# Performance work log

Hardware: AMD Instinct MI355X
Metric: run time of the kernel (lower is better)

## Reference

```python
import jax, jax.numpy as jnp
import numpy as np

N, E = 50000, 250000          # nodes, edges
IN, OUT, EDIM = 9, 84, 1      # NNConv(9, 84), edge nn Linear(1, 9*84)
EPS = 1e-5                    # BatchNorm1d default eps


def setup_inputs() -> dict:
    key = jax.random.key(0)
    ks = jax.random.split(key, 8)
    return {
        "x": jax.random.normal(ks[0], (N, IN), jnp.float32),
        "edge_index": jax.random.randint(ks[1], (2, E), 0, N, dtype=jnp.int64),
        "edge_attr": jax.random.normal(ks[2], (E, EDIM), jnp.float32),
        # edge nn: Linear(EDIM, IN*OUT) generating per-edge weight matrices
        "nn_w": jax.random.normal(ks[3], (EDIM, IN * OUT), jnp.float32) * (1.0 / np.sqrt(EDIM)),
        "nn_b": jnp.zeros((IN * OUT,), jnp.float32),
        # NNConv root weight + bias
        "root": jax.random.normal(ks[4], (IN, OUT), jnp.float32) * (1.0 / np.sqrt(IN)),
        "bias": jnp.zeros((OUT,), jnp.float32),
        # BatchNorm1d(84) affine params
        "gamma": jnp.ones((OUT,), jnp.float32),
        "beta": jnp.zeros((OUT,), jnp.float32),
    }


def reference(x, edge_index, edge_attr, nn_w, nn_b, root, bias, gamma, beta):
    src, dst = edge_index[0], edge_index[1]
    # per-edge weight matrices: [E, IN, OUT]
    w_e = (edge_attr @ nn_w + nn_b).reshape(E, IN, OUT)
    # gather source node features and apply edge-specific matmul: [E, OUT]
    msg = jnp.einsum('ei,eio->eo', x[src], w_e)
    # scatter-add to destination nodes (NNConv default aggr='add'): [N, OUT]
    aggr = jax.ops.segment_sum(msg, dst, num_segments=N)
    out = x @ root + aggr + bias
    # BatchNorm1d(84), training mode (biased batch stats)
    mean = out.mean(0)
    var = out.var(0)
    out = (out - mean) * jax.lax.rsqrt(var + EPS) * gamma + beta
    return out
```

## Files before the change

kernel.cpp:

```cpp
#include <hip/hip_runtime.h>

#define N_NODES 50000
#define E_EDGES 250000
#define IN_F 9
#define OUT_F 84
#define GROUPS 21
#define BN_EPS 1e-5f

#define NB_TILE 48
#define NTILES ((N_NODES + NB_TILE - 1) / NB_TILE)
#define NCOPIES 32
#define CAP 32

#define VDIM 27
#define NPAIR 378
#define NM 405
#define SLEN 408
#define VSTR 52
#define NSLOT 196

#define FB_TILE 96
#define FB_NT ((N_NODES + FB_TILE - 1) / FB_TILE)
#define VTS 28

#define CNT_OFF   0
#define STATC_OFF 50048
#define ZERO_WORDS 63104
#define SLOT_OFF  63232
#define SX_OFF    3263232
#define SS_OFF    4663232

__global__ __launch_bounds__(256)
void fill_slots_kernel(const int* __restrict__ ei,
                       const float* __restrict__ ea,
                       int* __restrict__ cnt,
                       int2* __restrict__ slot) {
    int e = (blockIdx.x * blockDim.x + threadIdx.x) * 4;
    if (e < E_EDGES) {
        int4   s4 = *(const int4*)&ei[e];
        int4   d4 = *(const int4*)&ei[E_EDGES + e];
        float4 a4 = *(const float4*)&ea[e];
        int pos;
        pos = atomicAdd(&cnt[d4.x], 1);
        if (pos < CAP) slot[d4.x * CAP + pos] = make_int2(s4.x, __float_as_int(a4.x));
        pos = atomicAdd(&cnt[d4.y], 1);
        if (pos < CAP) slot[d4.y * CAP + pos] = make_int2(s4.y, __float_as_int(a4.y));
        pos = atomicAdd(&cnt[d4.z], 1);
        if (pos < CAP) slot[d4.z * CAP + pos] = make_int2(s4.z, __float_as_int(a4.z));
        pos = atomicAdd(&cnt[d4.w], 1);
        if (pos < CAP) slot[d4.w * CAP + pos] = make_int2(s4.w, __float_as_int(a4.w));
    }
}

__global__ void gather_gram_kernel(const float* __restrict__ x,
                                   const int*   __restrict__ cnt,
                                   const int2*  __restrict__ slot,
                                   float* __restrict__ SX,
                                   float* __restrict__ statc) {
    __shared__ __align__(16) float V[VDIM * VSTR];
    __shared__ __align__(16) int2 rec[NB_TILE][CAP];
    __shared__ int cnt_s[NB_TILE];
    __shared__ unsigned char sI[NSLOT], sJ[NSLOT];

    const int tid = threadIdx.x;
    const int nbase = blockIdx.x * NB_TILE;

    for (int t = tid; t < NSLOT; t += blockDim.x) {
        int tt = t, i = 0;
        while (tt >= ((VDIM - i + 1) >> 1)) { tt -= (VDIM - i + 1) >> 1; ++i; }
        sI[t] = (unsigned char)i;
        sJ[t] = (unsigned char)(i + 2 * tt);
    }
    for (int t = tid; t < VDIM * 4; t += blockDim.x)
        V[(t >> 2) * VSTR + NB_TILE + (t & 3)] = 0.f;
    if (tid < NB_TILE) {
        int n = nbase + tid;
        int c = (n < N_NODES) ? cnt[n] : 0;
        cnt_s[tid] = (c > CAP) ? CAP : c;
    }
    __syncthreads();

    if (tid < NB_TILE * 4) {
        int nl = tid >> 2, part = tid & 3;
        int c = cnt_s[nl];
        const int4* grow = (const int4*)&slot[(nbase + nl) * CAP];
        int4* lrow = (int4*)&rec[nl][0];
#pragma unroll
        for (int j = 0; j < 4; ++j) {
            int s = part * 8 + j * 2;
            if (s < c) lrow[part * 4 + j] = grow[part * 4 + j];
        }
    }
    __syncthreads();

    for (int it = tid; it < NB_TILE * IN_F; it += blockDim.x) {
        int nl = it / IN_F, i = it - nl * IN_F;
        int n = nbase + nl;
        float xv = 0.f, s0 = 0.f, s1 = 0.f;
        if (n < N_NODES) {
            xv = x[n * IN_F + i];
            int c = cnt_s[nl];
            const int2* r = rec[nl];
            int k = 0;
            for (; k + 4 <= c; k += 4) {
                int2 r0 = r[k], r1 = r[k+1], r2 = r[k+2], r3 = r[k+3];
                float a0 = x[r0.x * IN_F + i];
                float a1 = x[r1.x * IN_F + i];
                float a2 = x[r2.x * IN_F + i];
                float a3 = x[r3.x * IN_F + i];
                s0 += (a0 + a1) + (a2 + a3);
                s1 += __int_as_float(r0.y) * a0 + __int_as_float(r1.y) * a1
                    + __int_as_float(r2.y) * a2 + __int_as_float(r3.y) * a3;
            }
            for (; k < c; ++k) {
                int2 r0 = r[k];
                float a0 = x[r0.x * IN_F + i];
                s0 += a0;
                s1 += __int_as_float(r0.y) * a0;
            }
            float* sx = SX + n * VTS;
            sx[i]      = xv;
            sx[9 + i]  = s0;
            sx[18 + i] = s1;
        }
        V[i * VSTR + nl]        = xv;
        V[(9 + i) * VSTR + nl]  = s0;
        V[(18 + i) * VSTR + nl] = s1;
    }
    __syncthreads();

    float* sc = statc + (blockIdx.x & (NCOPIES - 1)) * SLEN;
    for (int t = tid; t < NSLOT + VDIM; t += blockDim.x) {
        if (t < NSLOT) {
            int i = sI[t], j0 = sJ[t];
            int h2 = (j0 < VDIM - 1);
            const float4* vi = (const float4*)&V[i * VSTR];
            const float4* va = (const float4*)&V[j0 * VSTR];
            const float4* vb = (const float4*)&V[(j0 + h2) * VSTR];
            float acc0 = 0.f, acc1 = 0.f;
#pragma unroll
            for (int m = 0; m < VSTR / 4; ++m) {
                float4 a = vi[m], p = va[m], q = vb[m];
                acc0 += a.x * p.x + a.y * p.y + a.z * p.z + a.w * p.w;
                acc1 += a.x * q.x + a.y * q.y + a.z * q.z + a.w * q.w;
            }
            int base = i * VDIM - (i * (i - 1)) / 2;
            atomicAdd(&sc[base + (j0 - i)], acc0);
            if (h2) atomicAdd(&sc[base + (j0 - i) + 1], acc1);
        } else {
            int r = t - NSLOT;
            const float4* vi = (const float4*)&V[r * VSTR];
            float acc = 0.f;
#pragma unroll
            for (int m = 0; m < VSTR / 4; ++m) {
                float4 a = vi[m];
                acc += (a.x + a.y) + (a.z + a.w);
            }
            atomicAdd(&sc[NPAIR + r], acc);
        }
    }
}

__global__ __launch_bounds__(256)
void scale_kernel(const float* __restrict__ nw,
                  const float* __restrict__ nb,
                  const float* __restrict__ root,
                  const float* __restrict__ bias,
                  const float* __restrict__ gamma,
                  const float* __restrict__ beta,
                  const float* __restrict__ statc,
                  float* __restrict__ ss) {
    __shared__ float M[NM];
    const int tid = threadIdx.x;
    for (int t = tid; t < NM; t += blockDim.x) {
        float a = 0.f;
#pragma unroll
        for (int c = 0; c < NCOPIES; ++c) a += statc[c * SLEN + t];
        M[t] = a;
    }
    __syncthreads();
    if (tid < OUT_F) {
        const int o = tid;
        float c[VDIM];
#pragma unroll
        for (int i = 0; i < IN_F; ++i) {
            c[i]      = root[i * OUT_F + o];
            c[9 + i]  = nb[i * OUT_F + o];
            c[18 + i] = nw[i * OUT_F + o];
        }
        float sv = 0.f;
#pragma unroll
        for (int i = 0; i < VDIM; ++i) sv += M[NPAIR + i] * c[i];
        float q = 0.f;
        int t2 = 0;
        for (int i = 0; i < VDIM; ++i) {
            q += c[i] * c[i] * M[t2++];
            for (int j = i + 1; j < VDIM; ++j)
                q += 2.f * c[i] * c[j] * M[t2++];
        }
        const float b = bias[o];
        const float inv_n = 1.0f / (float)N_NODES;
        float mean  = (sv + (float)N_NODES * b) * inv_n;
        float sumsq = q + 2.f * b * sv + (float)N_NODES * b * b;
        float var   = sumsq * inv_n - mean * mean;
        float scl   = rsqrtf(var + BN_EPS) * gamma[o];
        ss[o]         = scl;
        ss[OUT_F + o] = beta[o] - mean * scl;
    }
}

__global__ __launch_bounds__(256, 2)
void final_kernel(const float* __restrict__ SX,
                  const float* __restrict__ nw,
                  const float* __restrict__ nb,
                  const float* __restrict__ root,
                  const float* __restrict__ bias,
                  const float* __restrict__ ss,
                  float* __restrict__ out) {
    __shared__ __align__(16) float4 Ws[IN_F * GROUPS];
    __shared__ __align__(16) float4 Bs[IN_F * GROUPS];
    __shared__ __align__(16) float4 Rs[IN_F * GROUPS];
    __shared__ __align__(16) float Vt[FB_TILE * VTS];

    const int tid = threadIdx.x;
    const int nbase = blockIdx.x * FB_TILE;
    const int nn = (N_NODES - nbase < FB_TILE) ? (N_NODES - nbase) : FB_TILE;

    for (int t = tid; t < IN_F * GROUPS; t += blockDim.x) {
        Ws[t] = ((const float4*)nw)[t];
        Bs[t] = ((const float4*)nb)[t];
        Rs[t] = ((const float4*)root)[t];
    }

    {
        const float4* sx4 = (const float4*)(SX + nbase * VTS);
        float4* vt4 = (float4*)Vt;
        const int nf4 = (nn * VTS) >> 2;
        for (int f = tid; f < nf4; f += blockDim.x)
            vt4[f] = sx4[f];
    }
    __syncthreads();

    const int g = tid % GROUPS;
    const int lane = tid / GROUPS;
    if (tid < 252) {
        float4 C[27];
#pragma unroll
        for (int i = 0; i < IN_F; ++i) {
            C[i]      = Rs[i * GROUPS + g];
            C[9 + i]  = Bs[i * GROUPS + g];
            C[18 + i] = Ws[i * GROUPS + g];
        }
        const float4 b4  = ((const float4*)bias)[g];
        const float4 sc4 = ((const float4*)ss)[g];
        const float4 sh4 = ((const float4*)(ss + OUT_F))[g];
#pragma unroll
        for (int k = 0; k < 8; ++k) {
            const int nl = k * 12 + lane;
            const int n  = nbase + nl;
            if (n < N_NODES) {
                const float* vr = &Vt[nl * VTS];
                float4 a0 = *(const float4*)(vr + 0);
                float4 a1 = *(const float4*)(vr + 4);
                float4 a2 = *(const float4*)(vr + 8);
                float4 a3 = *(const float4*)(vr + 12);
                float4 a4 = *(const float4*)(vr + 16);
                float4 a5 = *(const float4*)(vr + 20);
                float4 a6 = *(const float4*)(vr + 24);
                float4 acc = b4;
#define ACC(VC, IDX)                                                      \
                acc.x += (VC) * C[IDX].x;                                 \
                acc.y += (VC) * C[IDX].y;                                 \
                acc.z += (VC) * C[IDX].z;                                 \
                acc.w += (VC) * C[IDX].w;
                ACC(a0.x, 0)  ACC(a0.y, 1)  ACC(a0.z, 2)  ACC(a0.w, 3)
                ACC(a1.x, 4)  ACC(a1.y, 5)  ACC(a1.z, 6)  ACC(a1.w, 7)
                ACC(a2.x, 8)  ACC(a2.y, 9)  ACC(a2.z, 10) ACC(a2.w, 11)
                ACC(a3.x, 12) ACC(a3.y, 13) ACC(a3.z, 14) ACC(a3.w, 15)
                ACC(a4.x, 16) ACC(a4.y, 17) ACC(a4.z, 18) ACC(a4.w, 19)
                ACC(a5.x, 20) ACC(a5.y, 21) ACC(a5.z, 22) ACC(a5.w, 23)
                ACC(a6.x, 24) ACC(a6.y, 25) ACC(a6.z, 26)
#undef ACC
                acc.x = acc.x * sc4.x + sh4.x;
                acc.y = acc.y * sc4.y + sh4.y;
                acc.z = acc.z * sc4.z + sh4.z;
                acc.w = acc.w * sc4.w + sh4.w;
                *(float4*)&out[n * OUT_F + g * 4] = acc;
            }
        }
    }
}

extern "C" void kernel_launch(void* const* d_in, const int* in_sizes, int n_in,
                              void* d_out, int out_size, void* d_ws, size_t ws_size,
                              hipStream_t stream) {
    const float* x     = (const float*)d_in[0];
    const int*   ei    = (const int*)d_in[1];
    const float* ea    = (const float*)d_in[2];
    const float* nw    = (const float*)d_in[3];
    const float* nb    = (const float*)d_in[4];
    const float* root  = (const float*)d_in[5];
    const float* bias  = (const float*)d_in[6];
    const float* gamma = (const float*)d_in[7];
    const float* beta  = (const float*)d_in[8];
    float*       out   = (float*)d_out;

    float* wsf   = (float*)d_ws;
    int*   wsi   = (int*)d_ws;
    int*   cnt   = wsi + CNT_OFF;
    float* statc = wsf + STATC_OFF;
    int2*  slot  = (int2*)(wsi + SLOT_OFF);
    float* SX    = wsf + SX_OFF;
    float* ss    = wsf + SS_OFF;

    hipMemsetAsync(wsi, 0, ZERO_WORDS * sizeof(int), stream);
    fill_slots_kernel<<<(E_EDGES / 4 + 255) / 256, 256, 0, stream>>>(ei, ea, cnt, slot);
    gather_gram_kernel<<<NTILES, 256, 0, stream>>>(x, cnt, slot, SX, statc);
    scale_kernel<<<1, 256, 0, stream>>>(nw, nb, root, bias, gamma, beta, statc, ss);
    final_kernel<<<FB_NT, 256, 0, stream>>>(SX, nw, nb, root, bias, ss, out);
}
```

Baseline: 116.6 us.

## Pad x to 12 floats for float4 neighbor gathers and enlarge node tile

```diff
diff --git a/kernel.cpp b/kernel.cpp
--- a/kernel.cpp
+++ b/kernel.cpp
@@ -7,8 +7,6 @@
 #define GROUPS 21
 #define BN_EPS 1e-5f
 
-#define NB_TILE 48
-#define NTILES ((N_NODES + NB_TILE - 1) / NB_TILE)
 #define NCOPIES 32
 #define CAP 32
 
@@ -16,12 +14,18 @@
 #define NPAIR 378
 #define NM 405
 #define SLEN 408
-#define VSTR 52
 #define NSLOT 196
+
+#define NB2 96
+#define NT2 ((N_NODES + NB2 - 1) / NB2)
+#define VSTR2 100
 
 #define FB_TILE 96
 #define FB_NT ((N_NODES + FB_TILE - 1) / FB_TILE)
 #define VTS 28
+
+#define EB ((E_EDGES / 4 + 255) / 256)
+#define XB ((N_NODES + 255) / 256)
 
 #define CNT_OFF   0
 #define STATC_OFF 50048
@@ -29,41 +33,56 @@
 #define SLOT_OFF  63232
 #define SX_OFF    3263232
 #define SS_OFF    4663232
+#define XP_OFF    4663408
 
 __global__ __launch_bounds__(256)
 void fill_slots_kernel(const int* __restrict__ ei,
                        const float* __restrict__ ea,
+                       const float* __restrict__ x,
                        int* __restrict__ cnt,
-                       int2* __restrict__ slot) {
-    int e = (blockIdx.x * blockDim.x + threadIdx.x) * 4;
-    if (e < E_EDGES) {
-        int4   s4 = *(const int4*)&ei[e];
-        int4   d4 = *(const int4*)&ei[E_EDGES + e];
-        float4 a4 = *(const float4*)&ea[e];
-        int pos;
-        pos = atomicAdd(&cnt[d4.x], 1);
-        if (pos < CAP) slot[d4.x * CAP + pos] = make_int2(s4.x, __float_as_int(a4.x));
-        pos = atomicAdd(&cnt[d4.y], 1);
-        if (pos < CAP) slot[d4.y * CAP + pos] = make_int2(s4.y, __float_as_int(a4.y));
-        pos = atomicAdd(&cnt[d4.z], 1);
-        if (pos < CAP) slot[d4.z * CAP + pos] = make_int2(s4.z, __float_as_int(a4.z));
-        pos = atomicAdd(&cnt[d4.w], 1);
-        if (pos < CAP) slot[d4.w * CAP + pos] = make_int2(s4.w, __float_as_int(a4.w));
-    }
-}
-
-__global__ void gather_gram_kernel(const float* __restrict__ x,
-                                   const int*   __restrict__ cnt,
-                                   const int2*  __restrict__ slot,
-                                   float* __restrict__ SX,
-                                   float* __restrict__ statc) {
-    __shared__ __align__(16) float V[VDIM * VSTR];
-    __shared__ __align__(16) int2 rec[NB_TILE][CAP];
-    __shared__ int cnt_s[NB_TILE];
+                       int2* __restrict__ slot,
+                       float* __restrict__ xp) {
+    const int bx = blockIdx.x, tid = threadIdx.x;
+    if (bx < EB) {
+        int e = (bx * 256 + tid) * 4;
+        if (e < E_EDGES) {
+            int4   s4 = *(const int4*)&ei[e];
+            int4   d4 = *(const int4*)&ei[E_EDGES + e];
+            float4 a4 = *(const float4*)&ea[e];
+            int pos;
+            pos = atomicAdd(&cnt[d4.x], 1);
+            if (pos < CAP) slot[d4.x * CAP + pos] = make_int2(s4.x, __float_as_int(a4.x));
+            pos = atomicAdd(&cnt[d4.y], 1);
+            if (pos < CAP) slot[d4.y * CAP + pos] = make_int2(s4.y, __float_as_int(a4.y));
+            pos = atomicAdd(&cnt[d4.z], 1);
+            if (pos < CAP) slot[d4.z * CAP + pos] = make_int2(s4.z, __float_as_int(a4.z));
+            pos = atomicAdd(&cnt[d4.w], 1);
+            if (pos < CAP) slot[d4.w * CAP + pos] = make_int2(s4.w, __float_as_int(a4.w));
+        }
+    } else {
+        int n = (bx - EB) * 256 + tid;
+        if (n < N_NODES) {
+            const float* xr = x + n * IN_F;
+            float4* xd = (float4*)&xp[n * 12];
+            xd[0] = make_float4(xr[0], xr[1], xr[2], xr[3]);
+            xd[1] = make_float4(xr[4], xr[5], xr[6], xr[7]);
+            xd[2] = make_float4(xr[8], 0.f, 0.f, 0.f);
+        }
+    }
+}
+
+__global__ __launch_bounds__(256)
+void gather_gram_kernel(const float* __restrict__ xp,
+                        const int*   __restrict__ cnt,
+                        const int2*  __restrict__ slot,
+                        float* __restrict__ SX,
+                        float* __restrict__ statc) {
+    __shared__ __align__(16) float V[VDIM * VSTR2];
+    __shared__ int cnt_s[NB2];
     __shared__ unsigned char sI[NSLOT], sJ[NSLOT];
 
     const int tid = threadIdx.x;
-    const int nbase = blockIdx.x * NB_TILE;
+    const int nbase = blockIdx.x * NB2;
 
     for (int t = tid; t < NSLOT; t += blockDim.x) {
         int tt = t, i = 0;
@@ -72,60 +91,77 @@
         sJ[t] = (unsigned char)(i + 2 * tt);
     }
     for (int t = tid; t < VDIM * 4; t += blockDim.x)
-        V[(t >> 2) * VSTR + NB_TILE + (t & 3)] = 0.f;
-    if (tid < NB_TILE) {
+        V[(t >> 2) * VSTR2 + NB2 + (t & 3)] = 0.f;
+    if (tid < NB2) {
         int n = nbase + tid;
         int c = (n < N_NODES) ? cnt[n] : 0;
         cnt_s[tid] = (c > CAP) ? CAP : c;
     }
     __syncthreads();
 
-    if (tid < NB_TILE * 4) {
-        int nl = tid >> 2, part = tid & 3;
-        int c = cnt_s[nl];
-        const int4* grow = (const int4*)&slot[(nbase + nl) * CAP];
-        int4* lrow = (int4*)&rec[nl][0];
-#pragma unroll
-        for (int j = 0; j < 4; ++j) {
-            int s = part * 8 + j * 2;
-            if (s < c) lrow[part * 4 + j] = grow[part * 4 + j];
-        }
-    }
-    __syncthreads();
-
-    for (int it = tid; it < NB_TILE * IN_F; it += blockDim.x) {
-        int nl = it / IN_F, i = it - nl * IN_F;
+    const float4* xp4 = (const float4*)xp;
+    for (int it = tid; it < NB2 * 3; it += blockDim.x) {
+        int nl = it / 3, q = it - nl * 3;
         int n = nbase + nl;
-        float xv = 0.f, s0 = 0.f, s1 = 0.f;
+        float4 xq = make_float4(0.f, 0.f, 0.f, 0.f);
+        float4 s0 = xq, s1 = xq;
         if (n < N_NODES) {
-            xv = x[n * IN_F + i];
+            xq = xp4[n * 3 + q];
             int c = cnt_s[nl];
-            const int2* r = rec[nl];
+            const int2* r = &slot[n * CAP];
             int k = 0;
             for (; k + 4 <= c; k += 4) {
-                int2 r0 = r[k], r1 = r[k+1], r2 = r[k+2], r3 = r[k+3];
-                float a0 = x[r0.x * IN_F + i];
-                float a1 = x[r1.x * IN_F + i];
-                float a2 = x[r2.x * IN_F + i];
-                float a3 = x[r3.x * IN_F + i];
-                s0 += (a0 + a1) + (a2 + a3);
-                s1 += __int_as_float(r0.y) * a0 + __int_as_float(r1.y) * a1
-                    + __int_as_float(r2.y) * a2 + __int_as_float(r3.y) * a3;
+                int4 p0 = *(const int4*)&r[k];
+                int4 p1 = *(const int4*)&r[k + 2];
+                float4 a0 = xp4[p0.x * 3 + q];
+                float4 a1 = xp4[p0.z * 3 + q];
+                float4 a2 = xp4[p1.x * 3 + q];
+                float4 a3 = xp4[p1.z * 3 + q];
+                float w0 = __int_as_float(p0.y), w1 = __int_as_float(p0.w);
+                float w2 = __int_as_float(p1.y), w3 = __int_as_float(p1.w);
+                s0.x += (a0.x + a1.x) + (a2.x + a3.x);
+                s0.y += (a0.y + a1.y) + (a2.y + a3.y);
+                s0.z += (a0.z + a1.z) + (a2.z + a3.z);
+                s0.w += (a0.w + a1.w) + (a2.w + a3.w);
+                s1.x += w0 * a0.x + w1 * a1.x + w2 * a2.x + w3 * a3.x;
+                s1.y += w0 * a0.y + w1 * a1.y + w2 * a2.y + w3 * a3.y;
+                s1.z += w0 * a0.z + w1 * a1.z + w2 * a2.z + w3 * a3.z;
+                s1.w += w0 * a0.w + w1 * a1.w + w2 * a2.w + w3 * a3.w;
             }
             for (; k < c; ++k) {
                 int2 r0 = r[k];
-                float a0 = x[r0.x * IN_F + i];
-                s0 += a0;
-                s1 += __int_as_float(r0.y) * a0;
+                float4 a0 = xp4[r0.x * 3 + q];
+                float w0 = __int_as_float(r0.y);
+                s0.x += a0.x; s0.y += a0.y; s0.z += a0.z; s0.w += a0.w;
+                s1.x += w0 * a0.x; s1.y += w0 * a0.y;
+                s1.z += w0 * a0.z; s1.w += w0 * a0.w;
             }
             float* sx = SX + n * VTS;
-            sx[i]      = xv;
-            sx[9 + i]  = s0;
-            sx[18 + i] = s1;
-        }
-        V[i * VSTR + nl]        = xv;
-        V[(9 + i) * VSTR + nl]  = s0;
-        V[(18 + i) * VSTR + nl] = s1;
+            int f0 = q * 4;
+            sx[f0]      = xq.x;
+            sx[9 + f0]  = s0.x;
+            sx[18 + f0] = s1.x;
+            if (q < 2) {
+                sx[f0 + 1] = xq.y; sx[9 + f0 + 1] = s0.y; sx[18 + f0 + 1] = s1.y;
+                sx[f0 + 2] = xq.z; sx[9 + f0 + 2] = s0.z; sx[18 + f0 + 2] = s1.z;
+                sx[f0 + 3] = xq.w; sx[9 + f0 + 3] = s0.w; sx[18 + f0 + 3] = s1.w;
+            }
+        }
+        int f0 = q * 4;
+        V[f0 * VSTR2 + nl]        = xq.x;
+        V[(9 + f0) * VSTR2 + nl]  = s0.x;
+        V[(18 + f0) * VSTR2 + nl] = s1.x;
+        if (q < 2) {
+            V[(f0 + 1) * VSTR2 + nl]      = xq.y;
+            V[(9 + f0 + 1) * VSTR2 + nl]  = s0.y;
+            V[(18 + f0 + 1) * VSTR2 + nl] = s1.y;
+            V[(f0 + 2) * VSTR2 + nl]      = xq.z;
+            V[(9 + f0 + 2) * VSTR2 + nl]  = s0.z;
+            V[(18 + f0 + 2) * VSTR2 + nl] = s1.z;
+            V[(f0 + 3) * VSTR2 + nl]      = xq.w;
+            V[(9 + f0 + 3) * VSTR2 + nl]  = s0.w;
+            V[(18 + f0 + 3) * VSTR2 + nl] = s1.w;
+        }
     }
     __syncthreads();
 
@@ -134,25 +170,25 @@
         if (t < NSLOT) {
             int i = sI[t], j0 = sJ[t];
             int h2 = (j0 < VDIM - 1);
-            const float4* vi = (const float4*)&V[i * VSTR];
-            const float4* va = (const float4*)&V[j0 * VSTR];
-            const float4* vb = (const float4*)&V[(j0 + h2) * VSTR];
+            const float4* vi = (const float4*)&V[i * VSTR2];
+            const float4* va = (const float4*)&V[j0 * VSTR2];
+            const float4* vb = (const float4*)&V[(j0 + h2) * VSTR2];
             float acc0 = 0.f, acc1 = 0.f;
 #pragma unroll
-            for (int m = 0; m < VSTR / 4; ++m) {
-                float4 a = vi[m], p = va[m], q = vb[m];
+            for (int m = 0; m < VSTR2 / 4; ++m) {
+                float4 a = vi[m], p = va[m], q4 = vb[m];
                 acc0 += a.x * p.x + a.y * p.y + a.z * p.z + a.w * p.w;
-                acc1 += a.x * q.x + a.y * q.y + a.z * q.z + a.w * q.w;
+                acc1 += a.x * q4.x + a.y * q4.y + a.z * q4.z + a.w * q4.w;
             }
             int base = i * VDIM - (i * (i - 1)) / 2;
             atomicAdd(&sc[base + (j0 - i)], acc0);
             if (h2) atomicAdd(&sc[base + (j0 - i) + 1], acc1);
         } else {
             int r = t - NSLOT;
-            const float4* vi = (const float4*)&V[r * VSTR];
+            const float4* vi = (const float4*)&V[r * VSTR2];
             float acc = 0.f;
 #pragma unroll
-            for (int m = 0; m < VSTR / 4; ++m) {
+            for (int m = 0; m < VSTR2 / 4; ++m) {
                 float4 a = vi[m];
                 acc += (a.x + a.y) + (a.z + a.w);
             }
@@ -312,10 +348,11 @@
     int2*  slot  = (int2*)(wsi + SLOT_OFF);
     float* SX    = wsf + SX_OFF;
     float* ss    = wsf + SS_OFF;
+    float* xp    = wsf + XP_OFF;
 
     hipMemsetAsync(wsi, 0, ZERO_WORDS * sizeof(int), stream);
-    fill_slots_kernel<<<(E_EDGES / 4 + 255) / 256, 256, 0, stream>>>(ei, ea, cnt, slot);
-    gather_gram_kernel<<<NTILES, 256, 0, stream>>>(x, cnt, slot, SX, statc);
+    fill_slots_kernel<<<EB + XB, 256, 0, stream>>>(ei, ea, x, cnt, slot, xp);
+    gather_gram_kernel<<<NT2, 256, 0, stream>>>(xp, cnt, slot, SX, statc);
     scale_kernel<<<1, 256, 0, stream>>>(nw, nb, root, bias, gamma, beta, statc, ss);
     final_kernel<<<FB_NT, 256, 0, stream>>>(SX, nw, nb, root, bias, ss, out);
 }
```

Result: slower. 122.2 us (+4.9%).
